# Kernel optimization log

Measured on AMD Instinct MI355X. Metric: run time of the kernel, lower is better.

## Reference

```python
import jax, jax.numpy as jnp
import numpy as np

D_MODEL = 2048
NUM_HEADS = 16
HEAD_DIM = D_MODEL // NUM_HEADS


def _rotary(x, head_dim):
    # x: (..., T, head_dim). Matches torch module: half-split rotation.
    T = x.shape[-2]
    pos = jnp.arange(T, dtype=jnp.float32)[:, None]              # (T,1)
    dim = jnp.arange(head_dim // 2, dtype=jnp.float32)[None, :]  # (1,hd/2)
    angle = pos * (1.0 / jnp.power(10000.0, 2.0 * dim / head_dim))
    cos = jnp.cos(angle)  # (T, hd/2), broadcasts over leading dims
    sin = jnp.sin(angle)
    x1 = x[..., : head_dim // 2]
    x2 = x[..., head_dim // 2:]
    return jnp.concatenate([x1 * cos - x2 * sin, x2 * cos + x1 * sin], axis=-1)


def setup_inputs() -> dict:
    key = jax.random.key(0)
    ks = jax.random.split(key, 9)
    B, T, D, H, HD = 2, 2048, D_MODEL, NUM_HEADS, HEAD_DIM
    s = 1.0 / np.sqrt(D)
    return {
        "x": jax.random.normal(ks[0], (B, T, D), jnp.float32),
        "Wq": jax.random.normal(ks[1], (D, D), jnp.float32) * s,
        "bq": jnp.zeros((D,), jnp.float32),
        "Wk": jax.random.normal(ks[2], (D, HD), jnp.float32) * s,
        "bk": jnp.zeros((HD,), jnp.float32),
        "Wv": jax.random.normal(ks[3], (D, HD), jnp.float32) * s,
        "bv": jnp.zeros((HD,), jnp.float32),
        "Wo": jax.random.normal(ks[4], (D, D), jnp.float32) * s,
        "bo": jnp.zeros((D,), jnp.float32),
    }


def reference(x, Wq, bq, Wk, bk, Wv, bv, Wo, bo):
    B, T, D = x.shape
    H, HD = NUM_HEADS, HEAD_DIM
    q = (x @ Wq + bq).reshape(B, T, H, HD).transpose(0, 2, 1, 3)  # (B,H,T,hd)
    k = (x @ Wk + bk)[:, None]                                    # (B,1,T,hd)
    v = (x @ Wv + bv)[:, None]                                    # (B,1,T,hd)
    q = _rotary(q, HD)
    k = _rotary(k, HD)
    scores = jnp.einsum("bhqd,bhkd->bhqk", q, jnp.broadcast_to(k, (B, 1, T, HD))) / jnp.sqrt(jnp.float32(HD))
    attn = jax.nn.softmax(scores, axis=-1)                        # (B,H,T,T)
    ctx = jnp.einsum("bhqk,bhkd->bhqd", attn, jnp.broadcast_to(v, (B, 1, T, HD)))
    ctx = ctx.transpose(0, 2, 1, 3).reshape(B, T, D)
    return ctx @ Wo + bo
```

## Files before the change

### kernel.cpp

```cpp
#include <hip/hip_runtime.h>
#include <math.h>

#define T_SEQ  2048
#define DMODEL 2048
#define NHEADS 16
#define HDIM   128
#define MROWS  4096

typedef __attribute__((ext_vector_type(8)))  __bf16 bf16x8;
typedef __attribute__((ext_vector_type(4)))  __bf16 bf16x4;
typedef __attribute__((ext_vector_type(4)))  float  f32x4;
typedef __attribute__((ext_vector_type(16))) float  f32x16;

#define GLOBAL_AS __attribute__((address_space(1)))
#define LDS_AS    __attribute__((address_space(3)))
__device__ __forceinline__ void async_copy16(const __bf16* g, __bf16* l) {
  __builtin_amdgcn_global_load_lds((const GLOBAL_AS void*)g, (LDS_AS void*)l, 16, 0, 0);
}

__global__ void build_rope_kernel(float2* __restrict__ rope) {
  int idx = blockIdx.x * blockDim.x + threadIdx.x;
  int d = idx & 63, pos = idx >> 6;
  double freq = pow(10000.0, -(double)d / 64.0);
  double ang = (double)pos * freq;
  rope[idx] = make_float2((float)cos(ang), (float)sin(ang));
}

__global__ void cast_bf16_kernel(const float* __restrict__ in,
                                 __bf16* __restrict__ out, int n4) {
  int i = blockIdx.x * blockDim.x + threadIdx.x;
  if (i >= n4) return;
  float4 v = ((const float4*)in)[i];
  bf16x4 o = { (__bf16)v.x, (__bf16)v.y, (__bf16)v.z, (__bf16)v.w };
  *(bf16x4*)(out + (size_t)i*4) = o;
}

__global__ void wtrans_kernel(const float* __restrict__ Wq,
                              const float* __restrict__ Wk,
                              const float* __restrict__ Wv,
                              const float* __restrict__ Wo,
                              __bf16* __restrict__ wqkvt,
                              __bf16* __restrict__ wot) {
  __shared__ float t[32][33];
  const int bx = blockIdx.x;
  const float* src; __bf16* dst; int istride, c0, orow;
  if (bx < 64)       { src = Wq; istride = 2048; c0 = bx*32;      orow = c0;        dst = wqkvt; }
  else if (bx < 68)  { src = Wk; istride = 128;  c0 = (bx-64)*32; orow = 2048 + c0; dst = wqkvt; }
  else if (bx < 72)  { src = Wv; istride = 128;  c0 = (bx-68)*32; orow = 2176 + c0; dst = wqkvt; }
  else               { src = Wo; istride = 2048; c0 = (bx-72)*32; orow = c0;        dst = wot; }
  const int tx = threadIdx.x & 31, ty = threadIdx.x >> 5;
  const int r0 = blockIdx.y*32;
#pragma unroll
  for (int i = 0; i < 4; ++i)
    t[ty + i*8][tx] = src[(size_t)(r0 + ty + i*8)*istride + c0 + tx];
  __syncthreads();
#pragma unroll
  for (int i = 0; i < 4; ++i)
    dst[(size_t)(orow + ty + i*8)*2048 + r0 + tx] = (__bf16)t[tx][ty + i*8];
}

__global__ void transpose_v_kernel(const __bf16* __restrict__ in,
                                   __bf16* __restrict__ out) {
  __shared__ __bf16 t[32][34];
  const int bz = blockIdx.z;
  in  += (size_t)bz * 2048 * 128;
  out += (size_t)bz * 128 * 2048;
  const int tx = threadIdx.x & 31, ty = threadIdx.x >> 5;
  const int r0 = blockIdx.y*32, c0 = blockIdx.x*32;
#pragma unroll
  for (int i = 0; i < 4; ++i)
    t[ty + i*8][tx] = in[(size_t)(r0 + ty + i*8)*128 + c0 + tx];
  __syncthreads();
#pragma unroll
  for (int i = 0; i < 4; ++i)
    out[(size_t)(c0 + ty + i*8)*2048 + r0 + tx] = t[tx][ty + i*8];
}

__global__ __launch_bounds__(256) void gemm_qkv_fused(
    const __bf16* __restrict__ A,
    const __bf16* __restrict__ Bt,
    const float* __restrict__ bq, const float* __restrict__ bk,
    const float* __restrict__ bv,
    const float2* __restrict__ rope,
    __bf16* __restrict__ qrb,
    __bf16* __restrict__ kbb,
    __bf16* __restrict__ vbb,
    float qscale)
{
  __shared__ __bf16 As[128*32];
  __shared__ __bf16 Bs[128*32];
  const int tid = threadIdx.x;
  const int lane = tid & 63, wave = tid >> 6;
  const int quad = lane >> 4, l16 = lane & 15;
  const int m0 = (wave >> 1)*64, n0 = (wave & 1)*32;
  const int row0 = blockIdx.y*128, col0 = blockIdx.x*128;
  const int srow = lane >> 2, scol = (lane & 3)*8;

  f32x4 acc[4][4];
#pragma unroll
  for (int i = 0; i < 4; ++i)
#pragma unroll
    for (int j = 0; j < 4; ++j) acc[i][j] = (f32x4){0.f,0.f,0.f,0.f};

  const __bf16* Ag = A  + (size_t)(row0 + wave*32 + srow)*DMODEL + scol;
  const __bf16* Bg = Bt + (size_t)(col0 + wave*32 + srow)*DMODEL + scol;
  __bf16* AsW = &As[wave*1024];
  __bf16* BsW = &Bs[wave*1024];

  for (int kk = 0; kk < DMODEL; kk += 32) {
    __syncthreads();
    async_copy16(Ag + kk,                     AsW);
    async_copy16(Ag + kk + (size_t)16*DMODEL, AsW + 512);
    async_copy16(Bg + kk,                     BsW);
    async_copy16(Bg + kk + (size_t)16*DMODEL, BsW + 512);
    __syncthreads();
    bf16x8 af[4], bfr[4];
#pragma unroll
    for (int i = 0; i < 4; ++i)
      af[i] = *(const bf16x8*)&As[(m0 + i*16 + l16)*32 + quad*8];
#pragma unroll
    for (int j = 0; j < 4; ++j) {
      const int cb = n0 + (j & 1)*16 + (j >> 1)*64;
      bfr[j] = *(const bf16x8*)&Bs[(cb + l16)*32 + quad*8];
    }
#pragma unroll
    for (int i = 0; i < 4; ++i)
#pragma unroll
      for (int j = 0; j < 4; ++j)
        acc[i][j] = __builtin_amdgcn_mfma_f32_16x16x32_bf16(af[i], bfr[j], acc[i][j], 0,0,0);
  }

  const int bx = blockIdx.x;
  const float* bias_p; float scale; bool rot; __bf16* obase; int ostride;
  if (bx < 16)      { bias_p = bq + bx*128; scale = qscale; rot = true;
                      obase = qrb + bx*128; ostride = 2048; }
  else if (bx == 16){ bias_p = bk; scale = 1.f; rot = true;
                      obase = kbb; ostride = 128; }
  else              { bias_p = bv; scale = 1.f; rot = false;
                      obase = vbb; ostride = 128; }

#pragma unroll
  for (int j = 0; j < 2; ++j) {
    const int d = n0 + j*16 + l16;
    const float b1 = bias_p[d], b2 = bias_p[d + 64];
#pragma unroll
    for (int i = 0; i < 4; ++i) {
      const int rl = m0 + i*16 + quad*4;
#pragma unroll
      for (int r = 0; r < 4; ++r) {
        const int rg = row0 + rl + r;
        const float x1 = acc[i][j][r]   + b1;
        const float x2 = acc[i][j+2][r] + b2;
        float c = 1.f, s = 0.f;
        if (rot) { float2 cs = rope[(size_t)(rg & (T_SEQ-1))*64 + d]; c = cs.x; s = cs.y; }
        obase[(size_t)rg*ostride + d]      = (__bf16)((x1*c - x2*s)*scale);
        obase[(size_t)rg*ostride + d + 64] = (__bf16)((x2*c + x1*s)*scale);
      }
    }
  }
}

__global__ __launch_bounds__(256) void gemm_bf16_t128(
    const __bf16* __restrict__ A, const __bf16* __restrict__ Bt,
    const float* __restrict__ bias, float* __restrict__ C,
    int M, int N, int K)
{
  __shared__ __bf16 As[128*32];
  __shared__ __bf16 Bs[128*32];
  const int tid = threadIdx.x;
  const int lane = tid & 63, wave = tid >> 6;
  const int quad = lane >> 4, l16 = lane & 15;
  const int m0 = (wave & 1)*64, n0 = (wave >> 1)*64;
  const int row0 = blockIdx.y*128, col0 = blockIdx.x*128;
  const int srow = lane >> 2, scol = (lane & 3)*8;

  f32x4 acc[4][4];
#pragma unroll
  for (int i = 0; i < 4; ++i)
#pragma unroll
    for (int j = 0; j < 4; ++j) acc[i][j] = (f32x4){0.f,0.f,0.f,0.f};

  const __bf16* Ag = A  + (size_t)(row0 + wave*32 + srow)*K + scol;
  const __bf16* Bg = Bt + (size_t)(col0 + wave*32 + srow)*K + scol;
  __bf16* AsW = &As[wave*1024];
  __bf16* BsW = &Bs[wave*1024];

  for (int kk = 0; kk < K; kk += 32) {
    __syncthreads();
    async_copy16(Ag + kk,              AsW);
    async_copy16(Ag + kk + (size_t)16*K, AsW + 512);
    async_copy16(Bg + kk,              BsW);
    async_copy16(Bg + kk + (size_t)16*K, BsW + 512);
    __syncthreads();
    bf16x8 af[4], bfr[4];
#pragma unroll
    for (int i = 0; i < 4; ++i)
      af[i] = *(const bf16x8*)&As[(m0 + i*16 + l16)*32 + quad*8];
#pragma unroll
    for (int j = 0; j < 4; ++j)
      bfr[j] = *(const bf16x8*)&Bs[(n0 + j*16 + l16)*32 + quad*8];
#pragma unroll
    for (int i = 0; i < 4; ++i)
#pragma unroll
      for (int j = 0; j < 4; ++j)
        acc[i][j] = __builtin_amdgcn_mfma_f32_16x16x32_bf16(af[i], bfr[j], acc[i][j], 0,0,0);
  }
#pragma unroll
  for (int j = 0; j < 4; ++j) {
    const int ccol = col0 + n0 + j*16 + l16;
    const float bvv = bias[ccol];
#pragma unroll
    for (int i = 0; i < 4; ++i) {
      const int crow = row0 + m0 + i*16 + quad*4;
#pragma unroll
      for (int r = 0; r < 4; ++r)
        C[(size_t)(crow + r)*N + ccol] = acc[i][j][r] + bvv;
    }
  }
}

#define KSTR 136
#define VSTR 72
__global__ __launch_bounds__(256) void mqa_attn_mfma(
    const __bf16* __restrict__ qb,
    const __bf16* __restrict__ kb,
    const __bf16* __restrict__ vt,
    __bf16* __restrict__ ctx)
{
  __shared__ __bf16 Ks[64*KSTR];
  __shared__ __bf16 Vs[128*VSTR];
  const int tid = threadIdx.x, lane = tid & 63, wave = tid >> 6;
  const int h5 = lane >> 5, l32 = lane & 31;
  const int swr = (l32 & 19) | ((l32 & 4) << 1) | ((l32 & 8) >> 1);
  const int h = blockIdx.y, b = blockIdx.z;
  const int qbase = blockIdx.x*128 + wave*32;

  bf16x8 qf[8];
  const __bf16* qp = qb + ((size_t)b*T_SEQ + qbase + l32)*DMODEL + h*HDIM;
#pragma unroll
  for (int ds = 0; ds < 8; ++ds) qf[ds] = *(const bf16x8*)(qp + ds*16 + h5*8);

  f32x16 oacc[4];
#pragma unroll
  for (int g = 0; g < 4; ++g)
#pragma unroll
    for (int r = 0; r < 16; ++r) oacc[g][r] = 0.f;
  float lsum = 0.f;

  const __bf16* kbase = kb + (size_t)b*T_SEQ*HDIM;
  const __bf16* vbase = vt + (size_t)b*HDIM*T_SEQ;

  for (int kt = 0; kt < T_SEQ/64; ++kt) {
    __syncthreads();
#pragma unroll
    for (int i = 0; i < 4; ++i) {
      int idx = i*256 + tid;
      int key = idx >> 4, c = idx & 15;
      *(bf16x8*)&Ks[key*KSTR + c*8] =
          *(const bf16x8*)(kbase + (size_t)(kt*64 + key)*HDIM + c*8);
    }
#pragma unroll
    for (int i = 0; i < 4; ++i) {
      int idx = i*256 + tid;
      int d = idx >> 3, c = idx & 7;
      *(bf16x8*)&Vs[d*VSTR + c*8] =
          *(const bf16x8*)(vbase + (size_t)d*T_SEQ + kt*64 + c*8);
    }
    __syncthreads();

#pragma unroll
    for (int kg = 0; kg < 2; ++kg) {
      f32x16 sacc;
#pragma unroll
      for (int r = 0; r < 16; ++r) sacc[r] = 0.f;
#pragma unroll
      for (int ds = 0; ds < 8; ++ds) {
        bf16x8 kf = *(const bf16x8*)&Ks[(kg*32 + swr)*KSTR + ds*16 + h5*8];
        sacc = __builtin_amdgcn_mfma_f32_32x32x16_bf16(kf, qf[ds], sacc, 0,0,0);
      }
      bf16x8 pf[2];
#pragma unroll
      for (int r = 0; r < 16; ++r) {
        float p = __builtin_amdgcn_exp2f(sacc[r]);
        lsum += p;
        pf[r >> 3][r & 7] = (__bf16)p;
      }
#pragma unroll
      for (int ks = 0; ks < 2; ++ks)
#pragma unroll
        for (int g = 0; g < 4; ++g) {
          bf16x8 vf = *(const bf16x8*)&Vs[(g*32 + l32)*VSTR + kg*32 + ks*16 + h5*8];
          oacc[g] = __builtin_amdgcn_mfma_f32_32x32x16_bf16(vf, pf[ks], oacc[g], 0,0,0);
        }
    }
  }

  lsum += __shfl_xor(lsum, 32);
  const float inv = 1.f / lsum;

  __bf16* op = ctx + ((size_t)b*T_SEQ + qbase + l32)*DMODEL + h*HDIM;
#pragma unroll
  for (int g = 0; g < 4; ++g)
#pragma unroll
    for (int rq = 0; rq < 4; ++rq) {
      const int d = g*32 + rq*8 + h5*4;
      bf16x4 ov = { (__bf16)(oacc[g][rq*4+0]*inv), (__bf16)(oacc[g][rq*4+1]*inv),
                    (__bf16)(oacc[g][rq*4+2]*inv), (__bf16)(oacc[g][rq*4+3]*inv) };
      *(bf16x4*)&op[d] = ov;
    }
}

extern "C" void kernel_launch(void* const* d_in, const int* in_sizes, int n_in,
                              void* d_out, int out_size, void* d_ws, size_t ws_size,
                              hipStream_t stream) {
  const float* x  = (const float*)d_in[0];
  const float* Wq = (const float*)d_in[1];
  const float* bq = (const float*)d_in[2];
  const float* Wk = (const float*)d_in[3];
  const float* bk = (const float*)d_in[4];
  const float* Wv = (const float*)d_in[5];
  const float* bv = (const float*)d_in[6];
  const float* Wo = (const float*)d_in[7];
  const float* bo = (const float*)d_in[8];
  float* out = (float*)d_out;

  uint8_t* ws = (uint8_t*)d_ws;
  __bf16* qrb  = (__bf16*)(ws);
  __bf16* xb   = (__bf16*)(ws + 16777216);
  __bf16* wqkvt= (__bf16*)(ws + 33554432);
  __bf16* wot  = (__bf16*)(ws + 42991616);
  __bf16* kbb  = (__bf16*)(ws + 51380224);
  __bf16* vbb  = (__bf16*)(ws + 52428800);
  __bf16* vtb  = (__bf16*)(ws + 53477376);
  float2* rope = (float2*)(ws + 54525952);

  const float qscale = 1.4426950408889634f * 0.08838834764831845f;

  build_rope_kernel<<<512, 256, 0, stream>>>(rope);
  wtrans_kernel<<<dim3(136,64), 256, 0, stream>>>(Wq, Wk, Wv, Wo, wqkvt, wot);
  cast_bf16_kernel<<<8192, 256, 0, stream>>>(x, xb, MROWS*DMODEL/4);

  gemm_qkv_fused<<<dim3(18,32), 256, 0, stream>>>(
      xb, wqkvt, bq, bk, bv, rope, qrb, kbb, vbb, qscale);

  transpose_v_kernel<<<dim3(4,64,2), 256, 0, stream>>>(vbb, vtb);

  mqa_attn_mfma<<<dim3(16,16,2), 256, 0, stream>>>(qrb, kbb, vtb, xb);

  gemm_bf16_t128<<<dim3(16,32), 256, 0, stream>>>(xb, wot, bo, out, MROWS, DMODEL, DMODEL);
}
```

Baseline: 360.7 us.

## Prefetch next K/V tile into registers and split QK accumulators for MFMA ILP

The attention loop now loads the next K/V tile from global memory into registers while the current tile is being computed, then writes it to LDS at the start of the next iteration, so global load latency is hidden behind the MFMA work. The QK^T product is also split into four independent accumulator chains (two key groups times low/high head-dim halves) that are summed before exp, which removes serial MFMA dependencies. The cost is higher VGPR pressure from the prefetch registers and the extra accumulators, which may lower occupancy. The last iteration also issues one redundant wrap-around load.

```diff
diff --git a/kernel.cpp b/kernel.cpp
--- a/kernel.cpp
+++ b/kernel.cpp
@@ -250,49 +250,74 @@
   const __bf16* kbase = kb + (size_t)b*T_SEQ*HDIM;
   const __bf16* vbase = vt + (size_t)b*HDIM*T_SEQ;
 
-  for (int kt = 0; kt < T_SEQ/64; ++kt) {
+  const int kkey = tid >> 2;
+  const int kcol = (tid & 3)*32;
+
+  bf16x8 kreg[4], vreg[4];
+#pragma unroll
+  for (int i = 0; i < 4; ++i) {
+    int idx = i*256 + tid;
+    kreg[i] = *(const bf16x8*)(kbase + (size_t)(idx >> 4)*HDIM + (idx & 15)*8);
+    vreg[i] = *(const bf16x8*)(vbase + (size_t)(idx >> 3)*T_SEQ + (idx & 7)*8);
+  }
+
+  constexpr int NT = T_SEQ/64;
+  for (int kt = 0; kt < NT; ++kt) {
     __syncthreads();
 #pragma unroll
     for (int i = 0; i < 4; ++i) {
       int idx = i*256 + tid;
-      int key = idx >> 4, c = idx & 15;
-      *(bf16x8*)&Ks[key*KSTR + c*8] =
-          *(const bf16x8*)(kbase + (size_t)(kt*64 + key)*HDIM + c*8);
-    }
-#pragma unroll
-    for (int i = 0; i < 4; ++i) {
-      int idx = i*256 + tid;
-      int d = idx >> 3, c = idx & 7;
-      *(bf16x8*)&Vs[d*VSTR + c*8] =
-          *(const bf16x8*)(vbase + (size_t)d*T_SEQ + kt*64 + c*8);
-    }
-    __syncthreads();
-
-#pragma unroll
-    for (int kg = 0; kg < 2; ++kg) {
-      f32x16 sacc;
-#pragma unroll
-      for (int r = 0; r < 16; ++r) sacc[r] = 0.f;
-#pragma unroll
-      for (int ds = 0; ds < 8; ++ds) {
-        bf16x8 kf = *(const bf16x8*)&Ks[(kg*32 + swr)*KSTR + ds*16 + h5*8];
-        sacc = __builtin_amdgcn_mfma_f32_32x32x16_bf16(kf, qf[ds], sacc, 0,0,0);
+      *(bf16x8*)&Ks[(idx >> 4)*KSTR + (idx & 15)*8] = kreg[i];
+      *(bf16x8*)&Vs[(idx >> 3)*VSTR + (idx & 7)*8]  = vreg[i];
+    }
+    __syncthreads();
+    {
+      const int ktn = (kt + 1 < NT) ? kt + 1 : 0;
+#pragma unroll
+      for (int i = 0; i < 4; ++i) {
+        int idx = i*256 + tid;
+        kreg[i] = *(const bf16x8*)(kbase + (size_t)(ktn*64 + (idx >> 4))*HDIM + (idx & 15)*8);
+        vreg[i] = *(const bf16x8*)(vbase + (size_t)(idx >> 3)*T_SEQ + ktn*64 + (idx & 7)*8);
       }
-      bf16x8 pf[2];
+    }
+
+    f32x16 s_lo[2], s_hi[2];
+#pragma unroll
+    for (int kg = 0; kg < 2; ++kg)
+#pragma unroll
+      for (int r = 0; r < 16; ++r) { s_lo[kg][r] = 0.f; s_hi[kg][r] = 0.f; }
+#pragma unroll
+    for (int ds = 0; ds < 4; ++ds) {
+      bf16x8 k00 = *(const bf16x8*)&Ks[swr*KSTR        + ds*16 + h5*8];
+      bf16x8 k01 = *(const bf16x8*)&Ks[(32+swr)*KSTR   + ds*16 + h5*8];
+      bf16x8 k10 = *(const bf16x8*)&Ks[swr*KSTR        + (ds+4)*16 + h5*8];
+      bf16x8 k11 = *(const bf16x8*)&Ks[(32+swr)*KSTR   + (ds+4)*16 + h5*8];
+      s_lo[0] = __builtin_amdgcn_mfma_f32_32x32x16_bf16(k00, qf[ds],   s_lo[0], 0,0,0);
+      s_lo[1] = __builtin_amdgcn_mfma_f32_32x32x16_bf16(k01, qf[ds],   s_lo[1], 0,0,0);
+      s_hi[0] = __builtin_amdgcn_mfma_f32_32x32x16_bf16(k10, qf[ds+4], s_hi[0], 0,0,0);
+      s_hi[1] = __builtin_amdgcn_mfma_f32_32x32x16_bf16(k11, qf[ds+4], s_hi[1], 0,0,0);
+    }
+
+    bf16x8 pf[2][2];
+#pragma unroll
+    for (int kg = 0; kg < 2; ++kg)
 #pragma unroll
       for (int r = 0; r < 16; ++r) {
-        float p = __builtin_amdgcn_exp2f(sacc[r]);
+        float p = __builtin_amdgcn_exp2f(s_lo[kg][r] + s_hi[kg][r]);
         lsum += p;
-        pf[r >> 3][r & 7] = (__bf16)p;
+        pf[kg][r >> 3][r & 7] = (__bf16)p;
       }
-#pragma unroll
-      for (int ks = 0; ks < 2; ++ks)
+
+#pragma unroll
+    for (int kg = 0; kg < 2; ++kg)
+#pragma unroll
+      for (int ks = 0; ks < 2; ++ks) {
 #pragma unroll
         for (int g = 0; g < 4; ++g) {
           bf16x8 vf = *(const bf16x8*)&Vs[(g*32 + l32)*VSTR + kg*32 + ks*16 + h5*8];
-          oacc[g] = __builtin_amdgcn_mfma_f32_32x32x16_bf16(vf, pf[ks], oacc[g], 0,0,0);
+          oacc[g] = __builtin_amdgcn_mfma_f32_32x32x16_bf16(vf, pf[kg][ks], oacc[g], 0,0,0);
         }
-    }
+      }
   }
 
   lsum += __shfl_xor(lsum, 32);
```

After: 322.4 us. -10.6%, faster.
